# Kernel optimization log

Measured on AMD Instinct MI355X. Metric: run time of the kernel, lower is better.

Reference implementation:

```python
import jax, jax.numpy as jnp
import numpy as np

SIGMA_INIT = 1000.0


def setup_inputs() -> dict:
    key = jax.random.key(0)
    k1, k2, k3 = jax.random.split(key, 3)
    B, M, D, S = 1024, 209, 12288, 2
    input_data = jax.random.normal(k1, (B, D), dtype=jnp.float32)
    center = jax.random.normal(k2, (M, D), dtype=jnp.float32)
    sigma = SIGMA_INIT * jnp.ones((M,), dtype=jnp.float32)
    W = 50.0 * jax.random.normal(k3, (S, M), dtype=jnp.float32)
    b = jnp.zeros((S,), dtype=jnp.float32)
    return {"input_data": input_data, "center": center, "sigma": sigma, "W": W, "b": b}


def reference(input_data, center, sigma, W, b):
    # Euclidean distance ||x_i - c_j|| via GEMM expansion (avoids [B,M,D] diff tensor)
    x2 = jnp.sum(input_data * input_data, axis=1, keepdims=True)        # [B,1]
    c2 = jnp.sum(center * center, axis=1)[None, :]                      # [1,M]
    d2 = x2 + c2 - 2.0 * (input_data @ center.T)                        # [B,M]
    dist = jnp.sqrt(jnp.maximum(d2, 0.0))
    # Note: original divides the (non-squared) norm by sigma^2, then exp(-.)
    radial = jnp.exp(-dist / (sigma * sigma)[None, :])                  # [B,M]
    return radial @ W.T + b                                             # [B,S]
```

## Files before the change

### kernel.cpp

```cpp
#include <hip/hip_runtime.h>
#include <hip/hip_bf16.h>
#include <stdint.h>

#define B_SZ 1024
#define M_SZ 209
#define MPAD 224
#define D_SZ 12288
#define KC   32
#define KCH  384
#define BK   128
#define NIT  (KCH / BK)
#define NB   32
#define BT   32
#define NCT  7
#define SROW 224
#define SLROW (KC * SROW)

#define CBF_OFF  0u
#define XXP_OFF  (MPAD * D_SZ)
#define CCP_OFF  (XXP_OFF + B_SZ * KC * 4)
#define SLAB_OFF (CCP_OFF + MPAD * 2 * 4)

typedef __attribute__((ext_vector_type(8))) short short8;
typedef __attribute__((ext_vector_type(4))) float floatx4;

__device__ __forceinline__ uint32_t pk8x4(const float4& v) {
    int d = __builtin_amdgcn_cvt_pk_fp8_f32(v.x, v.y, 0, false);
    d     = __builtin_amdgcn_cvt_pk_fp8_f32(v.z, v.w, d, true);
    return (uint32_t)d;
}

__device__ __forceinline__ float bfbits2f(unsigned short u) {
    union { uint32_t u; float f; } cv;
    cv.u = ((uint32_t)u) << 16;
    return cv.f;
}

__device__ __forceinline__ void gload_lds16(const void* g, void* l) {
    __builtin_amdgcn_global_load_lds(
        (const __attribute__((address_space(1))) void*)g,
        (__attribute__((address_space(3))) void*)l, 16, 0, 0);
}

__global__ __launch_bounds__(256) void rbf_prep(
    const float* __restrict__ c, uint8_t* __restrict__ cf8,
    float* __restrict__ ccp)
{
    __shared__ float red[4];
    const int j = blockIdx.x >> 1, h = blockIdx.x & 1;
    const int t = threadIdx.x;
    const int base = h * (D_SZ / 2);
    uint8_t* dst = cf8 + (size_t)j * D_SZ + base;
    float s = 0.f;
    if (j < M_SZ) {
        const float* src = c + (size_t)j * D_SZ + base;
        for (int i = t * 8; i < D_SZ / 2; i += 2048) {
            float4 v0 = *(const float4*)(src + i);
            float4 v1 = *(const float4*)(src + i + 4);
            s += v0.x*v0.x + v0.y*v0.y + v0.z*v0.z + v0.w*v0.w
               + v1.x*v1.x + v1.y*v1.y + v1.z*v1.z + v1.w*v1.w;
            uint2 w = { pk8x4(v0), pk8x4(v1) };
            *(uint2*)(dst + i) = w;
        }
    } else {
        uint2 zz = {0u, 0u};
        for (int i = t * 8; i < D_SZ / 2; i += 2048) *(uint2*)(dst + i) = zz;
    }
#pragma unroll
    for (int off = 32; off > 0; off >>= 1) s += __shfl_down(s, off);
    if ((t & 63) == 0) red[t >> 6] = s;
    __syncthreads();
    if (t == 0) ccp[j * 2 + h] = red[0] + red[1] + red[2] + red[3];
}

__global__ __launch_bounds__(256, 4) void rbf_main(
    const float* __restrict__ x, const uint8_t* __restrict__ cf8,
    __hip_bfloat16* __restrict__ slab, float* __restrict__ xxp)
{
    __shared__ uint8_t sx[BT * BK];
    __shared__ uint8_t sc[MPAD * BK];

    const int t    = threadIdx.x;
    const int k    = blockIdx.x;
    const int b    = blockIdx.y;
    const int wave = t >> 6, lane = t & 63;
    const int quad = lane >> 4, mrow = lane & 15;
    const int qh = quad >> 1, ql = quad & 1;
    const int s2 = (mrow >> 1) & 7;
    const int rt  = wave & 1;
    const int cth = wave >> 1;

    floatx4 acc[NCT];
    const floatx4 z4 = {0.f, 0.f, 0.f, 0.f};
#pragma unroll
    for (int i = 0; i < NCT; ++i) acc[i] = z4;

    const int oE = (((lane & 7) ^ (lane >> 4)) & 7) * 16;
    const int oO = ((((lane & 7) ^ (lane >> 4)) ^ 4) & 7) * 16;
    const uint8_t* cpbE = cf8 + (size_t)(lane >> 3) * D_SZ + (size_t)k * KCH + oE;
    const uint8_t* cpbO = cf8 + (size_t)(lane >> 3) * D_SZ + (size_t)k * KCH + oO;

#pragma unroll
    for (int jj = 0; jj < 7; ++jj) {
        const int cr = wave * 7 + jj;
        const uint8_t* p = ((cr & 1) ? cpbO : cpbE) + (size_t)cr * 8 * D_SZ;
        gload_lds16(p, &sc[cr * 1024]);
    }

    const int xr = t >> 3;
    const int xc = t & 7;
    const float* xp = x + (size_t)(b * BT + xr) * D_SZ + (size_t)k * KCH + xc * 16;

    uint4 xw[NIT];
    float sxx = 0.f;
#pragma unroll
    for (int it = 0; it < NIT; ++it) {
        float4 v0 = *(const float4*)(xp + it * BK + 0);
        float4 v1 = *(const float4*)(xp + it * BK + 4);
        float4 v2 = *(const float4*)(xp + it * BK + 8);
        float4 v3 = *(const float4*)(xp + it * BK + 12);
        sxx += v0.x*v0.x + v0.y*v0.y + v0.z*v0.z + v0.w*v0.w
             + v1.x*v1.x + v1.y*v1.y + v1.z*v1.z + v1.w*v1.w
             + v2.x*v2.x + v2.y*v2.y + v2.z*v2.z + v2.w*v2.w
             + v3.x*v3.x + v3.y*v3.y + v3.z*v3.z + v3.w*v3.w;
        xw[it] = make_uint4(pk8x4(v0), pk8x4(v1), pk8x4(v2), pk8x4(v3));
    }
    uint8_t* sxw = &sx[xr * BK + ((xc ^ ((xr >> 1) & 7)) & 7) * 16];

    int boff[4];
#pragma unroll
    for (int ks = 0; ks < 4; ++ks)
        boff[ks] = (((ks * 2 + qh) ^ s2) & 7) * 16 + ql * 8;
    const uint8_t* abase = &sx[(rt * 16 + mrow) * BK];
    const uint8_t* bbase = &sc[(cth * 7 * 16 + mrow) * BK];

    for (int it = 0; it < NIT; ++it) {
        *(uint4*)sxw = xw[it];
        __syncthreads();
#pragma unroll
        for (int ks = 0; ks < 4; ++ks) {
            const long a = *(const long*)(abase + boff[ks]);
#pragma unroll
            for (int ct = 0; ct < NCT; ++ct) {
                const long bv = *(const long*)(bbase + ct * 16 * BK + boff[ks]);
                acc[ct] = __builtin_amdgcn_mfma_f32_16x16x32_fp8_fp8(a, bv, acc[ct], 0, 0, 0);
            }
        }
        __syncthreads();
        if (it + 1 < NIT) {
#pragma unroll
            for (int jj = 0; jj < 7; ++jj) {
                const int cr = wave * 7 + jj;
                const uint8_t* p = ((cr & 1) ? cpbO : cpbE)
                                 + (size_t)cr * 8 * D_SZ + (it + 1) * BK;
                gload_lds16(p, &sc[cr * 1024]);
            }
        }
    }

    __hip_bfloat16* sd = slab + (size_t)k * SROW;
    const int gi0 = b * BT + rt * 16 + quad * 4;
#pragma unroll
    for (int ct = 0; ct < NCT; ++ct) {
        const int gj = (cth * 7 + ct) * 16 + mrow;
#pragma unroll
        for (int rg = 0; rg < 4; ++rg)
            sd[(size_t)(gi0 + rg) * SLROW + gj] = __float2bfloat16(acc[ct][rg]);
    }

    sxx += __shfl_down(sxx, 4);
    sxx += __shfl_down(sxx, 2);
    sxx += __shfl_down(sxx, 1);
    if ((t & 7) == 0) xxp[(size_t)(b * BT + xr) * KC + k] = sxx;
}

__global__ __launch_bounds__(256) void rbf_fin(
    const __hip_bfloat16* __restrict__ slab, const float* __restrict__ xxp,
    const float* __restrict__ ccp, const float* __restrict__ sigma,
    const float* __restrict__ W, const float* __restrict__ bias,
    float* __restrict__ out)
{
    __shared__ float jpart[MPAD * 9];
    __shared__ float jtot[MPAD];
    __shared__ float xsh;

    const int t = threadIdx.x;
    const int i = blockIdx.x;

    if (t < 64) {
        float xv = (t < KC) ? xxp[(size_t)i * KC + t] : 0.f;
#pragma unroll
        for (int off = 32; off > 0; off >>= 1) xv += __shfl_down(xv, off);
        if (t == 0) xsh = xv;
    }

    const int o = t % 28, g = t / 28;
    if (t < 252) {
        const unsigned short* sp = (const unsigned short*)slab
                                 + (size_t)i * SLROW + o * 8;
        float s8[8] = {0.f,0.f,0.f,0.f,0.f,0.f,0.f,0.f};
        for (int kk = g; kk < KC; kk += 9) {
            short8 v = *(const short8*)(sp + kk * SROW);
#pragma unroll
            for (int e = 0; e < 8; ++e) s8[e] += bfbits2f((unsigned short)v[e]);
        }
#pragma unroll
        for (int e = 0; e < 8; ++e) jpart[(o * 8 + e) * 9 + g] = s8[e];
    }
    __syncthreads();

    if (t < MPAD) {
        float d = 0.f;
#pragma unroll
        for (int g2 = 0; g2 < 9; ++g2) d += jpart[t * 9 + g2];
        jtot[t] = d;
    }
    __syncthreads();

    if (t < 64) {
        const float xxi = xsh;
        float a0 = 0.f, a1 = 0.f;
        for (int j = t; j < M_SZ; j += 64) {
            const float ccj = ccp[j * 2] + ccp[j * 2 + 1];
            float d2 = fmaxf(xxi + ccj - 2.f * jtot[j], 0.f);
            float sg = sigma[j];
            float rad = __expf(-sqrtf(d2) / (sg * sg));
            a0 += rad * W[j];
            a1 += rad * W[M_SZ + j];
        }
#pragma unroll
        for (int off = 32; off > 0; off >>= 1) {
            a0 += __shfl_down(a0, off);
            a1 += __shfl_down(a1, off);
        }
        if (t == 0) {
            out[i * 2 + 0] = a0 + bias[0];
            out[i * 2 + 1] = a1 + bias[1];
        }
    }
}

extern "C" void kernel_launch(void* const* d_in, const int* in_sizes, int n_in,
                              void* d_out, int out_size, void* d_ws, size_t ws_size,
                              hipStream_t stream)
{
    const float* x     = (const float*)d_in[0];
    const float* c     = (const float*)d_in[1];
    const float* sigma = (const float*)d_in[2];
    const float* W     = (const float*)d_in[3];
    const float* bias  = (const float*)d_in[4];
    float* out = (float*)d_out;

    char* ws = (char*)d_ws;
    uint8_t*        cf8  = (uint8_t*)(ws + CBF_OFF);
    float*          xxp  = (float*)(ws + XXP_OFF);
    float*          ccp  = (float*)(ws + CCP_OFF);
    __hip_bfloat16* slab = (__hip_bfloat16*)(ws + SLAB_OFF);

    rbf_prep<<<MPAD * 2, 256, 0, stream>>>(c, cf8, ccp);
    rbf_main<<<dim3(KC, NB), 256, 0, stream>>>(x, cf8, slab, xxp);
    rbf_fin<<<B_SZ, 256, 0, stream>>>(slab, xxp, ccp, sigma, W, bias, out);
}
```

Before: 110.0 us.

## Pre-layout centers in MFMA fragment order and drop LDS staging in main GEMM

The prep kernel now writes the fp8 centers in a tiled layout that matches the MFMA B-fragment order, so each lane in the main kernel loads its operand straight from global memory with one coalesced 8-byte read. The main kernel no longer uses LDS or __syncthreads. Each lane converts its own x fragment in registers and double-buffers the center fragments in registers across 12 k-groups. This removes the LDS traffic and barriers, but the centers are now read redundantly by the waves that share a column tile, and more registers are live. The prep grid is halved to one block per center row.

Measured after the change: 127.1 us. 1.16x slower.

```diff
diff --git a/kernel.cpp b/kernel.cpp
--- a/kernel.cpp
+++ b/kernel.cpp
@@ -5,21 +5,22 @@
 #define B_SZ 1024
 #define M_SZ 209
 #define MPAD 224
+#define NTILE 14
 #define D_SZ 12288
 #define KC   32
 #define KCH  384
-#define BK   128
-#define NIT  (KCH / BK)
+#define KG   12
+#define KGTOT (D_SZ / 32)
 #define NB   32
 #define BT   32
 #define NCT  7
 #define SROW 224
 #define SLROW (KC * SROW)
 
-#define CBF_OFF  0u
-#define XXP_OFF  (MPAD * D_SZ)
-#define CCP_OFF  (XXP_OFF + B_SZ * KC * 4)
-#define SLAB_OFF (CCP_OFF + MPAD * 2 * 4)
+#define CT_OFF   0u
+#define XXP_OFF  (KGTOT * NTILE * 512)
+#define CC_OFF   (XXP_OFF + B_SZ * KC * 4)
+#define SLAB_OFF (CC_OFF + 1024)
 
 typedef __attribute__((ext_vector_type(8))) short short8;
 typedef __attribute__((ext_vector_type(4))) float floatx4;
@@ -36,147 +37,113 @@
     return cv.f;
 }
 
-__device__ __forceinline__ void gload_lds16(const void* g, void* l) {
-    __builtin_amdgcn_global_load_lds(
-        (const __attribute__((address_space(1))) void*)g,
-        (__attribute__((address_space(3))) void*)l, 16, 0, 0);
-}
-
 __global__ __launch_bounds__(256) void rbf_prep(
-    const float* __restrict__ c, uint8_t* __restrict__ cf8,
-    float* __restrict__ ccp)
+    const float* __restrict__ c, uint8_t* __restrict__ cT,
+    float* __restrict__ cc)
 {
     __shared__ float red[4];
-    const int j = blockIdx.x >> 1, h = blockIdx.x & 1;
-    const int t = threadIdx.x;
-    const int base = h * (D_SZ / 2);
-    uint8_t* dst = cf8 + (size_t)j * D_SZ + base;
+    const int j = blockIdx.x, t = threadIdx.x;
+    const int ct = j >> 4, mrow = j & 15;
     float s = 0.f;
-    if (j < M_SZ) {
-        const float* src = c + (size_t)j * D_SZ + base;
-        for (int i = t * 8; i < D_SZ / 2; i += 2048) {
-            float4 v0 = *(const float4*)(src + i);
-            float4 v1 = *(const float4*)(src + i + 4);
-            s += v0.x*v0.x + v0.y*v0.y + v0.z*v0.z + v0.w*v0.w
-               + v1.x*v1.x + v1.y*v1.y + v1.z*v1.z + v1.w*v1.w;
-            uint2 w = { pk8x4(v0), pk8x4(v1) };
-            *(uint2*)(dst + i) = w;
-        }
-    } else {
-        uint2 zz = {0u, 0u};
-        for (int i = t * 8; i < D_SZ / 2; i += 2048) *(uint2*)(dst + i) = zz;
+    for (int kg = t; kg < KGTOT; kg += 256) {
+        uint8_t* dst = cT + ((size_t)kg * NTILE + ct) * 512 + mrow * 8;
+        if (j < M_SZ) {
+            const float* src = c + (size_t)j * D_SZ + kg * 32;
+#pragma unroll
+            for (int q = 0; q < 4; ++q) {
+                float4 a = *(const float4*)(src + q * 8);
+                float4 b = *(const float4*)(src + q * 8 + 4);
+                s += a.x*a.x + a.y*a.y + a.z*a.z + a.w*a.w
+                   + b.x*b.x + b.y*b.y + b.z*b.z + b.w*b.w;
+                uint2 w = { pk8x4(a), pk8x4(b) };
+                *(uint2*)(dst + q * 128) = w;
+            }
+        } else {
+            const uint2 z = {0u, 0u};
+#pragma unroll
+            for (int q = 0; q < 4; ++q) *(uint2*)(dst + q * 128) = z;
+        }
     }
 #pragma unroll
     for (int off = 32; off > 0; off >>= 1) s += __shfl_down(s, off);
     if ((t & 63) == 0) red[t >> 6] = s;
     __syncthreads();
-    if (t == 0) ccp[j * 2 + h] = red[0] + red[1] + red[2] + red[3];
+    if (t == 0) cc[j] = red[0] + red[1] + red[2] + red[3];
 }
 
 __global__ __launch_bounds__(256, 4) void rbf_main(
-    const float* __restrict__ x, const uint8_t* __restrict__ cf8,
+    const float* __restrict__ x, const uint8_t* __restrict__ cT,
     __hip_bfloat16* __restrict__ slab, float* __restrict__ xxp)
 {
-    __shared__ uint8_t sx[BT * BK];
-    __shared__ uint8_t sc[MPAD * BK];
-
     const int t    = threadIdx.x;
     const int k    = blockIdx.x;
     const int b    = blockIdx.y;
     const int wave = t >> 6, lane = t & 63;
     const int quad = lane >> 4, mrow = lane & 15;
-    const int qh = quad >> 1, ql = quad & 1;
-    const int s2 = (mrow >> 1) & 7;
-    const int rt  = wave & 1;
-    const int cth = wave >> 1;
+    const int rt   = wave & 1;
+    const int cth  = wave >> 1;
 
     floatx4 acc[NCT];
     const floatx4 z4 = {0.f, 0.f, 0.f, 0.f};
 #pragma unroll
     for (int i = 0; i < NCT; ++i) acc[i] = z4;
 
-    const int oE = (((lane & 7) ^ (lane >> 4)) & 7) * 16;
-    const int oO = ((((lane & 7) ^ (lane >> 4)) ^ 4) & 7) * 16;
-    const uint8_t* cpbE = cf8 + (size_t)(lane >> 3) * D_SZ + (size_t)k * KCH + oE;
-    const uint8_t* cpbO = cf8 + (size_t)(lane >> 3) * D_SZ + (size_t)k * KCH + oO;
-
-#pragma unroll
-    for (int jj = 0; jj < 7; ++jj) {
-        const int cr = wave * 7 + jj;
-        const uint8_t* p = ((cr & 1) ? cpbO : cpbE) + (size_t)cr * 8 * D_SZ;
-        gload_lds16(p, &sc[cr * 1024]);
-    }
-
-    const int xr = t >> 3;
-    const int xc = t & 7;
-    const float* xp = x + (size_t)(b * BT + xr) * D_SZ + (size_t)k * KCH + xc * 16;
-
-    uint4 xw[NIT];
+    const float* xr = x + (size_t)(b * BT + rt * 16 + mrow) * D_SZ
+                    + (size_t)k * KCH + quad * 8;
+    long xa[KG];
     float sxx = 0.f;
 #pragma unroll
-    for (int it = 0; it < NIT; ++it) {
-        float4 v0 = *(const float4*)(xp + it * BK + 0);
-        float4 v1 = *(const float4*)(xp + it * BK + 4);
-        float4 v2 = *(const float4*)(xp + it * BK + 8);
-        float4 v3 = *(const float4*)(xp + it * BK + 12);
-        sxx += v0.x*v0.x + v0.y*v0.y + v0.z*v0.z + v0.w*v0.w
-             + v1.x*v1.x + v1.y*v1.y + v1.z*v1.z + v1.w*v1.w
-             + v2.x*v2.x + v2.y*v2.y + v2.z*v2.z + v2.w*v2.w
-             + v3.x*v3.x + v3.y*v3.y + v3.z*v3.z + v3.w*v3.w;
-        xw[it] = make_uint4(pk8x4(v0), pk8x4(v1), pk8x4(v2), pk8x4(v3));
-    }
-    uint8_t* sxw = &sx[xr * BK + ((xc ^ ((xr >> 1) & 7)) & 7) * 16];
-
-    int boff[4];
-#pragma unroll
-    for (int ks = 0; ks < 4; ++ks)
-        boff[ks] = (((ks * 2 + qh) ^ s2) & 7) * 16 + ql * 8;
-    const uint8_t* abase = &sx[(rt * 16 + mrow) * BK];
-    const uint8_t* bbase = &sc[(cth * 7 * 16 + mrow) * BK];
-
-    for (int it = 0; it < NIT; ++it) {
-        *(uint4*)sxw = xw[it];
-        __syncthreads();
-#pragma unroll
-        for (int ks = 0; ks < 4; ++ks) {
-            const long a = *(const long*)(abase + boff[ks]);
-#pragma unroll
-            for (int ct = 0; ct < NCT; ++ct) {
-                const long bv = *(const long*)(bbase + ct * 16 * BK + boff[ks]);
-                acc[ct] = __builtin_amdgcn_mfma_f32_16x16x32_fp8_fp8(a, bv, acc[ct], 0, 0, 0);
-            }
-        }
-        __syncthreads();
-        if (it + 1 < NIT) {
-#pragma unroll
-            for (int jj = 0; jj < 7; ++jj) {
-                const int cr = wave * 7 + jj;
-                const uint8_t* p = ((cr & 1) ? cpbO : cpbE)
-                                 + (size_t)cr * 8 * D_SZ + (it + 1) * BK;
-                gload_lds16(p, &sc[cr * 1024]);
-            }
-        }
+    for (int kg = 0; kg < KG; ++kg) {
+        float4 a = *(const float4*)(xr + kg * 32);
+        float4 bv = *(const float4*)(xr + kg * 32 + 4);
+        sxx += a.x*a.x + a.y*a.y + a.z*a.z + a.w*a.w
+             + bv.x*bv.x + bv.y*bv.y + bv.z*bv.z + bv.w*bv.w;
+        const uint32_t lo = pk8x4(a);
+        const uint32_t hi = pk8x4(bv);
+        xa[kg] = (long)(((uint64_t)hi << 32) | lo);
+    }
+
+    const uint8_t* bp = cT + ((size_t)(k * KG) * NTILE + cth * NCT) * 512 + lane * 8;
+
+    long bf[2][NCT];
+#pragma unroll
+    for (int ct = 0; ct < NCT; ++ct)
+        bf[0][ct] = *(const long*)(bp + ct * 512);
+
+#pragma unroll
+    for (int kg = 0; kg < KG; ++kg) {
+        const int cur = kg & 1, nxt = cur ^ 1;
+        if (kg + 1 < KG) {
+            const uint8_t* np = bp + (size_t)(kg + 1) * NTILE * 512;
+#pragma unroll
+            for (int ct = 0; ct < NCT; ++ct)
+                bf[nxt][ct] = *(const long*)(np + ct * 512);
+        }
+        const long a = xa[kg];
+#pragma unroll
+        for (int ct = 0; ct < NCT; ++ct)
+            acc[ct] = __builtin_amdgcn_mfma_f32_16x16x32_fp8_fp8(a, bf[cur][ct], acc[ct], 0, 0, 0);
     }
 
     __hip_bfloat16* sd = slab + (size_t)k * SROW;
     const int gi0 = b * BT + rt * 16 + quad * 4;
 #pragma unroll
     for (int ct = 0; ct < NCT; ++ct) {
-        const int gj = (cth * 7 + ct) * 16 + mrow;
+        const int gj = (cth * NCT + ct) * 16 + mrow;
 #pragma unroll
         for (int rg = 0; rg < 4; ++rg)
             sd[(size_t)(gi0 + rg) * SLROW + gj] = __float2bfloat16(acc[ct][rg]);
     }
 
-    sxx += __shfl_down(sxx, 4);
-    sxx += __shfl_down(sxx, 2);
-    sxx += __shfl_down(sxx, 1);
-    if ((t & 7) == 0) xxp[(size_t)(b * BT + xr) * KC + k] = sxx;
+    sxx += __shfl_down(sxx, 32);
+    sxx += __shfl_down(sxx, 16);
+    if (cth == 0 && lane < 16)
+        xxp[(size_t)(b * BT + rt * 16 + lane) * KC + k] = sxx;
 }
 
 __global__ __launch_bounds__(256) void rbf_fin(
     const __hip_bfloat16* __restrict__ slab, const float* __restrict__ xxp,
-    const float* __restrict__ ccp, const float* __restrict__ sigma,
+    const float* __restrict__ cc, const float* __restrict__ sigma,
     const float* __restrict__ W, const float* __restrict__ bias,
     float* __restrict__ out)
 {
@@ -221,8 +188,7 @@
         const float xxi = xsh;
         float a0 = 0.f, a1 = 0.f;
         for (int j = t; j < M_SZ; j += 64) {
-            const float ccj = ccp[j * 2] + ccp[j * 2 + 1];
-            float d2 = fmaxf(xxi + ccj - 2.f * jtot[j], 0.f);
+            float d2 = fmaxf(xxi + cc[j] - 2.f * jtot[j], 0.f);
             float sg = sigma[j];
             float rad = __expf(-sqrtf(d2) / (sg * sg));
             a0 += rad * W[j];
@@ -252,12 +218,12 @@
     float* out = (float*)d_out;
 
     char* ws = (char*)d_ws;
-    uint8_t*        cf8  = (uint8_t*)(ws + CBF_OFF);
+    uint8_t*        cT   = (uint8_t*)(ws + CT_OFF);
     float*          xxp  = (float*)(ws + XXP_OFF);
-    float*          ccp  = (float*)(ws + CCP_OFF);
+    float*          cc   = (float*)(ws + CC_OFF);
     __hip_bfloat16* slab = (__hip_bfloat16*)(ws + SLAB_OFF);
 
-    rbf_prep<<<MPAD * 2, 256, 0, stream>>>(c, cf8, ccp);
-    rbf_main<<<dim3(KC, NB), 256, 0, stream>>>(x, cf8, slab, xxp);
-    rbf_fin<<<B_SZ, 256, 0, stream>>>(slab, xxp, ccp, sigma, W, bias, out);
-}
+    rbf_prep<<<MPAD, 256, 0, stream>>>(c, cT, cc);
+    rbf_main<<<dim3(KC, NB), 256, 0, stream>>>(x, cT, slab, xxp);
+    rbf_fin<<<B_SZ, 256, 0, stream>>>(slab, xxp, cc, sigma, W, bias, out);
+}
```
